# Kernel tuning notes

Hardware: AMD Instinct MI355X
Metric: run time of the kernel (lower is better)

The kernel has to match this reference:

```python
import jax, jax.numpy as jnp
import numpy as np

B, D = 8192, 1024          # batch, input dim
UNITS = [1024, 512]        # expert MLP hidden sizes
T, E_T, E_S = 2, 2, 4      # num_tasks, experts per task, shared experts
E = T * E_T + E_S          # total experts = 8


def setup_inputs() -> dict:
    key = jax.random.key(0)
    k = jax.random.split(key, 6)
    H, O = UNITS
    x = jax.random.normal(k[0], (B, D), dtype=jnp.float32)
    # glorot-normal-ish scaling for expert weights
    W1 = jax.random.normal(k[1], (E, D, H), dtype=jnp.float32) * np.sqrt(2.0 / (D + H))
    b1 = jnp.zeros((E, H), dtype=jnp.float32)
    W2 = jax.random.normal(k[2], (E, H, O), dtype=jnp.float32) * np.sqrt(2.0 / (H + O))
    b2 = jnp.zeros((E, O), dtype=jnp.float32)
    # per-task gate over (E_T + E_S) experts, no bias (use_bias=False in Dense)
    Wg = jax.random.normal(k[3], (T, D, E_T + E_S), dtype=jnp.float32) * np.sqrt(2.0 / (D + E_T + E_S))
    # shared gate over all E experts
    Wgs = jax.random.normal(k[4], (D, E), dtype=jnp.float32) * np.sqrt(2.0 / (D + E))
    return {"x": x, "W1": W1, "b1": b1, "W2": W2, "b2": b2, "Wg": Wg, "Wgs": Wgs}


def reference(x, W1, b1, W2, b2, Wg, Wgs):
    # All experts see the same input (2D-input path of CGC3: tf.tile over experts).
    # Batched grouped GEMM over the expert axis instead of a Python loop.
    h = jax.nn.relu(jnp.einsum('bd,edh->ebh', x, W1) + b1[:, None, :])   # [E,B,H]
    eo = jax.nn.relu(jnp.einsum('ebh,eho->ebo', h, W2) + b2[:, None, :]) # [E,B,O]

    outs = []
    for i in range(T):
        # experts for task i = its own E_T experts + the last E_S shared experts
        idx = jnp.array(list(range(i * E_T, (i + 1) * E_T)) + list(range(E - E_S, E)))
        g = jax.nn.softmax(x @ Wg[i], axis=-1)            # [B, E_T+E_S]
        sel = eo[idx]                                     # [E_T+E_S, B, O]
        outs.append(jnp.einsum('be,ebo->bo', g, sel))     # [B, O]
    # output_share=True: share tower gated over all experts
    gs = jax.nn.softmax(x @ Wgs, axis=-1)                 # [B, E]
    outs.append(jnp.einsum('be,ebo->bo', gs, eo))         # [B, O]
    return jnp.stack(outs, axis=1)                        # [B, T+1, O]
```

## Files before the change

kernel.cpp:

```cpp
#include <hip/hip_runtime.h>
#include <hip/hip_bf16.h>
#include <stdint.h>

#define B_SZ 8192
#define D_SZ 1024
#define H_SZ 1024
#define O_SZ 512
#define E_SZ 8

typedef float f32x4 __attribute__((ext_vector_type(4)));
typedef __bf16 bf16x8 __attribute__((ext_vector_type(8)));

typedef __attribute__((address_space(1))) uint32_t gu32;
typedef __attribute__((address_space(3))) uint32_t lu32;

__device__ __forceinline__ unsigned short f2bf(float f) {
    union { __hip_bfloat16 h; unsigned short u; } c;
    c.h = __float2bfloat16(f);
    return c.u;
}
__device__ __forceinline__ float bf2f(unsigned short u) {
    union { float f; uint32_t u; } c;
    c.u = ((uint32_t)u) << 16;
    return c.f;
}

__global__ __launch_bounds__(256) void k_convert(const float* __restrict__ in,
                                                 unsigned short* __restrict__ out, int n8) {
    int i = blockIdx.x * 256 + threadIdx.x;
    if (i >= n8) return;
    const float4* p = (const float4*)in + (size_t)i * 2;
    float4 a = p[0], b = p[1];
    ushort4 lo, hi;
    lo.x = f2bf(a.x); lo.y = f2bf(a.y); lo.z = f2bf(a.z); lo.w = f2bf(a.w);
    hi.x = f2bf(b.x); hi.y = f2bf(b.y); hi.z = f2bf(b.z); hi.w = f2bf(b.w);
    ushort4* q = (ushort4*)out + (size_t)i * 2;
    q[0] = lo; q[1] = hi;
}

__global__ __launch_bounds__(512) void k_transpose_convert(const float* __restrict__ in,
                                                           unsigned short* __restrict__ out,
                                                           int R, int C) {
    __shared__ float tile[64][65];
    const float* src = in + (size_t)blockIdx.z * R * C;
    unsigned short* dst = out + (size_t)blockIdx.z * R * C;
    int c0 = blockIdx.x * 64, r0 = blockIdx.y * 64;
    int tx = threadIdx.x, ty = threadIdx.y;
#pragma unroll
    for (int rr = ty; rr < 64; rr += 8)
        tile[rr][tx] = src[(size_t)(r0 + rr) * C + c0 + tx];
    __syncthreads();
#pragma unroll
    for (int rr = ty; rr < 64; rr += 8)
        dst[(size_t)(c0 + rr) * R + r0 + tx] = f2bf(tile[tx][rr]);
}

__global__ __launch_bounds__(256) void k_gates(const float* __restrict__ x,
                                               const float* __restrict__ Wg,
                                               const float* __restrict__ Wgs,
                                               float* __restrict__ g_all) {
    const int wv = threadIdx.x >> 6;
    const int lane = threadIdx.x & 63;
    const int b = blockIdx.x * 4 + wv;
    const float* xr = x + (size_t)b * D_SZ;
    float acc[20];
#pragma unroll
    for (int j = 0; j < 20; ++j) acc[j] = 0.f;
    for (int d = lane; d < D_SZ; d += 64) {
        float xv = xr[d];
        const float* w0 = Wg + (size_t)d * 6;
        const float* w1 = Wg + (size_t)D_SZ * 6 + (size_t)d * 6;
        const float* ws = Wgs + (size_t)d * 8;
#pragma unroll
        for (int j = 0; j < 6; ++j) acc[j] += xv * w0[j];
#pragma unroll
        for (int j = 0; j < 6; ++j) acc[6 + j] += xv * w1[j];
#pragma unroll
        for (int j = 0; j < 8; ++j) acc[12 + j] += xv * ws[j];
    }
#pragma unroll
    for (int j = 0; j < 20; ++j) {
        float v = acc[j];
#pragma unroll
        for (int s = 32; s > 0; s >>= 1) v += __shfl_down(v, s, 64);
        acc[j] = v;
    }
    if (lane == 0) {
        float* g = g_all + (size_t)b * 20;
#pragma unroll
        for (int t = 0; t < 3; ++t) {
            int base = (t == 0) ? 0 : (t == 1 ? 6 : 12);
            int cnt  = (t == 2) ? 8 : 6;
            float m = -1e30f;
            for (int j = 0; j < cnt; ++j) m = fmaxf(m, acc[base + j]);
            float ex[8]; float sum = 0.f;
            for (int j = 0; j < cnt; ++j) { ex[j] = __expf(acc[base + j] - m); sum += ex[j]; }
            float inv = 1.f / sum;
            for (int j = 0; j < cnt; ++j) g[base + j] = ex[j] * inv;
        }
    }
}

__global__ __launch_bounds__(512, 2) void k_gemm4(
    const unsigned short* __restrict__ A,
    const unsigned short* __restrict__ Bt,
    const float* __restrict__ bias,
    unsigned short* __restrict__ C,
    int M, int N, int K,
    long long sA, long long sB, long long sBias, long long sC, int e_base) {

    const int tid = threadIdx.x;
    const int lane = tid & 63, wid = tid >> 6;
    const int wr = wid >> 2, wc = wid & 3;
    const int lr = lane & 15, lg = lane >> 4;

    const int nwg = gridDim.x;
    const int wg = blockIdx.x;
    const int swz = (wg & 7) * (nwg >> 3) + (wg >> 3);
    const int nx = N >> 8;
    const int my = M >> 8;
    const int bx = swz % nx;
    const int t1 = swz / nx;
    const int by = t1 % my;
    const int e  = t1 / my + e_base;

    A    += (size_t)((long long)e * sA);
    Bt   += (size_t)((long long)e * sB);
    bias += (size_t)((long long)e * sBias);
    C    += (size_t)((long long)e * sC);

    const int m0 = by * 256, n0 = bx * 256;

    __shared__ __align__(16) unsigned short lds[65536];
    char* ldsb = (char*)lds;

    const int srow = tid >> 2;
    const int scol = (((tid & 3) ^ ((tid >> 3) & 3)) * 8);
    const int sdst = tid * 16;

    auto stageA = [&](int t) {
        const int bb = (t & 3) * 32768;
        const unsigned short* s0 = A + (size_t)(m0 + srow) * K + (t << 5) + scol;
        __builtin_amdgcn_global_load_lds((gu32*)s0, (lu32*)(ldsb + bb + sdst), 16, 0, 0);
        __builtin_amdgcn_global_load_lds((gu32*)(s0 + (size_t)128 * K),
                                         (lu32*)(ldsb + bb + 8192 + sdst), 16, 0, 0);
    };
    auto stageB = [&](int t) {
        const int bb = (t & 3) * 32768 + 16384;
        const unsigned short* s0 = Bt + (size_t)(n0 + srow) * K + (t << 5) + scol;
        __builtin_amdgcn_global_load_lds((gu32*)s0, (lu32*)(ldsb + bb + sdst), 16, 0, 0);
        __builtin_amdgcn_global_load_lds((gu32*)(s0 + (size_t)128 * K),
                                         (lu32*)(ldsb + bb + 8192 + sdst), 16, 0, 0);
    };

    const int cblk = (lg ^ ((lr >> 1) & 3)) * 16;
    const int aoff = wr * 8192 + lr * 64 + cblk;
    const int boff = 16384 + (wc >> 1) * 8192 + (wc & 1) * 4096 + lr * 64 + cblk;

    auto loadf = [&](bf16x8* f, int bb) {
#pragma unroll
        for (int i = 0; i < 8; ++i)
            f[i] = *(const bf16x8*)(ldsb + bb + aoff + i * 1024);
#pragma unroll
        for (int j = 0; j < 4; ++j)
            f[8 + j] = *(const bf16x8*)(ldsb + bb + boff + j * 1024);
    };

    f32x4 acc[8][4];
#pragma unroll
    for (int i = 0; i < 8; ++i)
#pragma unroll
        for (int j = 0; j < 4; ++j)
            acc[i][j] = f32x4{0.f, 0.f, 0.f, 0.f};

    auto domfma = [&](const bf16x8* f) {
        __builtin_amdgcn_s_setprio(1);
#pragma unroll
        for (int i = 0; i < 8; ++i)
#pragma unroll
            for (int j = 0; j < 4; ++j)
                acc[i][j] = __builtin_amdgcn_mfma_f32_16x16x32_bf16(f[i], f[8 + j], acc[i][j], 0, 0, 0);
        __builtin_amdgcn_s_setprio(0);
    };

    const int NT = K >> 5;

    stageA(0); stageB(0); stageA(1); stageB(1); stageA(2); stageB(2);
    asm volatile("s_waitcnt vmcnt(4)" ::: "memory");
    asm volatile("s_barrier" ::: "memory");

    bf16x8 fA[12], fB[12];
    loadf(fA, 0);

    for (int t = 0; t < NT; t += 2) {
        if (t + 3 < NT) { stageA(t + 3); stageB(t + 3); }
        loadf(fB, ((t + 1) & 3) * 32768);
        domfma(fA);
        if (t + 3 < NT)      { asm volatile("s_waitcnt vmcnt(4)" ::: "memory"); }
        else if (t + 2 < NT) { asm volatile("s_waitcnt vmcnt(0)" ::: "memory"); }
        asm volatile("s_barrier" ::: "memory");

        if (t + 4 < NT) { stageA(t + 4); stageB(t + 4); }
        if (t + 2 < NT) loadf(fA, ((t + 2) & 3) * 32768);
        domfma(fB);
        if (t + 4 < NT)      { asm volatile("s_waitcnt vmcnt(4)" ::: "memory"); }
        else if (t + 3 < NT) { asm volatile("s_waitcnt vmcnt(0)" ::: "memory"); }
        asm volatile("s_barrier" ::: "memory");
    }

    unsigned short* ct = (unsigned short*)ldsb;
#pragma unroll
    for (int j = 0; j < 4; ++j) {
        const int nn = wc * 64 + j * 16 + lr;
        const float bv = bias[n0 + nn];
#pragma unroll
        for (int i = 0; i < 8; ++i) {
            const int mb = wr * 128 + i * 16 + lg * 4;
#pragma unroll
            for (int r = 0; r < 4; ++r) {
                float v = fmaxf(acc[i][j][r] + bv, 0.f);
                ct[(size_t)(mb + r) * 256 + nn] = f2bf(v);
            }
        }
    }
    __syncthreads();
#pragma unroll
    for (int it = 0; it < 16; ++it) {
        const int row = it * 16 + (tid >> 5);
        const int colE = (tid & 31) * 8;
        *(int4*)(&C[(size_t)(m0 + row) * N + n0 + colE]) =
            *(const int4*)(ldsb + it * 8192 + (size_t)tid * 16);
    }
}

__global__ __launch_bounds__(256) void k_combine(const unsigned short* __restrict__ eo,
                                                 const float* __restrict__ g_all,
                                                 float* __restrict__ out) {
    int idx4 = blockIdx.x * 256 + threadIdx.x;
    int b = idx4 >> 7;
    int o4 = (idx4 & 127) * 4;
    const float* g = g_all + (size_t)b * 20;
    float v[E_SZ][4];
#pragma unroll
    for (int e = 0; e < E_SZ; ++e) {
        ushort4 u = *(const ushort4*)(eo + (size_t)e * B_SZ * O_SZ + (size_t)b * O_SZ + o4);
        v[e][0] = bf2f(u.x); v[e][1] = bf2f(u.y); v[e][2] = bf2f(u.z); v[e][3] = bf2f(u.w);
    }
    float4 r0, r1, r2;
    float* p0 = (float*)&r0; float* p1 = (float*)&r1; float* p2 = (float*)&r2;
#pragma unroll
    for (int c = 0; c < 4; ++c) {
        p0[c] = g[0] * v[0][c] + g[1] * v[1][c] + g[2] * v[4][c] + g[3] * v[5][c]
              + g[4] * v[6][c] + g[5] * v[7][c];
        p1[c] = g[6] * v[2][c] + g[7] * v[3][c] + g[8] * v[4][c] + g[9] * v[5][c]
              + g[10] * v[6][c] + g[11] * v[7][c];
        float s = 0.f;
#pragma unroll
        for (int e = 0; e < E_SZ; ++e) s += g[12 + e] * v[e][c];
        p2[c] = s;
    }
    size_t ob = (size_t)b * (3 * O_SZ) + o4;
    *(float4*)(out + ob) = r0;
    *(float4*)(out + ob + O_SZ) = r1;
    *(float4*)(out + ob + 2 * O_SZ) = r2;
}

extern "C" void kernel_launch(void* const* d_in, const int* in_sizes, int n_in,
                              void* d_out, int out_size, void* d_ws, size_t ws_size,
                              hipStream_t stream) {
    const float* x   = (const float*)d_in[0];
    const float* W1  = (const float*)d_in[1];
    const float* b1  = (const float*)d_in[2];
    const float* W2  = (const float*)d_in[3];
    const float* b2  = (const float*)d_in[4];
    const float* Wg  = (const float*)d_in[5];
    const float* Wgs = (const float*)d_in[6];
    float* out = (float*)d_out;

    char* ws = (char*)d_ws;
    const size_t SZ_XBF  = (size_t)B_SZ * D_SZ * 2;
    const size_t SZ_W1T  = (size_t)E_SZ * H_SZ * D_SZ * 2;
    const size_t SZ_W2T  = (size_t)E_SZ * O_SZ * H_SZ * 2;
    const size_t SZ_EO   = (size_t)E_SZ * B_SZ * O_SZ * 2;
    const size_t SZ_G    = (size_t)B_SZ * 20 * 4;
    const size_t SZ_HBIG = (size_t)E_SZ * B_SZ * H_SZ * 2;

    unsigned short* x_bf = (unsigned short*)ws;              ws += SZ_XBF;
    unsigned short* W1T  = (unsigned short*)ws;              ws += SZ_W1T;
    unsigned short* W2T  = (unsigned short*)ws;              ws += SZ_W2T;
    unsigned short* eo   = (unsigned short*)ws;              ws += SZ_EO;
    float* g_all         = (float*)ws;                       ws += SZ_G;
    unsigned short* h_buf = (unsigned short*)ws;

    const size_t fixed = SZ_XBF + SZ_W1T + SZ_W2T + SZ_EO + SZ_G;
    const bool big = ws_size >= fixed + SZ_HBIG;

    k_convert<<<(B_SZ * D_SZ / 8 + 255) / 256, 256, 0, stream>>>(x, x_bf, B_SZ * D_SZ / 8);
    dim3 tb(64, 8);
    k_transpose_convert<<<dim3(H_SZ / 64, D_SZ / 64, E_SZ), tb, 0, stream>>>(W1, W1T, D_SZ, H_SZ);
    k_transpose_convert<<<dim3(O_SZ / 64, H_SZ / 64, E_SZ), tb, 0, stream>>>(W2, W2T, H_SZ, O_SZ);

    k_gates<<<B_SZ / 4, 256, 0, stream>>>(x, Wg, Wgs, g_all);

    if (big) {
        k_gemm4<<<(H_SZ / 256) * (B_SZ / 256) * E_SZ, 512, 0, stream>>>(
            x_bf, W1T, b1, h_buf, B_SZ, H_SZ, D_SZ,
            0LL, (long long)H_SZ * D_SZ, (long long)H_SZ, (long long)B_SZ * H_SZ, 0);
        k_gemm4<<<(O_SZ / 256) * (B_SZ / 256) * E_SZ, 512, 0, stream>>>(
            h_buf, W2T, b2, eo, B_SZ, O_SZ, H_SZ,
            (long long)B_SZ * H_SZ, (long long)O_SZ * H_SZ, (long long)O_SZ, (long long)B_SZ * O_SZ, 0);
    } else {
        for (int e = 0; e < E_SZ; ++e) {
            k_gemm4<<<(H_SZ / 256) * (B_SZ / 256), 512, 0, stream>>>(
                x_bf, W1T, b1, h_buf, B_SZ, H_SZ, D_SZ,
                0LL, (long long)H_SZ * D_SZ, (long long)H_SZ, 0LL, e);
            k_gemm4<<<(O_SZ / 256) * (B_SZ / 256), 512, 0, stream>>>(
                h_buf, W2T, b2, eo, B_SZ, O_SZ, H_SZ,
                0LL, (long long)O_SZ * H_SZ, (long long)O_SZ, (long long)B_SZ * O_SZ, e);
        }
    }

    k_combine<<<(B_SZ * O_SZ / 4) / 256, 256, 0, stream>>>(eo, g_all, out);
}
```

Before: 305.7 us.

## Switch GEMM to 32x32x16 MFMA tiles and fuse x conversion into gate kernel

The GEMM inner product moves from 16x16x32 MFMA instructions to 32x32x16 ones, with the fragment loads, accumulator layout and epilogue row mapping reworked to match. Larger MFMA tiles cut the instruction count and the LDS fragment reads per FLOP. Separately, the bf16 conversion of x is folded into the gate kernel, so x is read once and one launch is removed. The new epilogue index mapping must match the 32x32 output layout exactly, and the gate loop now reads x with float4 loads.

```diff
diff --git a/kernel.cpp b/kernel.cpp
--- a/kernel.cpp
+++ b/kernel.cpp
@@ -9,6 +9,7 @@
 #define E_SZ 8
 
 typedef float f32x4 __attribute__((ext_vector_type(4)));
+typedef float f32x16 __attribute__((ext_vector_type(16)));
 typedef __bf16 bf16x8 __attribute__((ext_vector_type(8)));
 
 typedef __attribute__((address_space(1))) uint32_t gu32;
@@ -25,58 +26,41 @@
     return c.f;
 }
 
-__global__ __launch_bounds__(256) void k_convert(const float* __restrict__ in,
-                                                 unsigned short* __restrict__ out, int n8) {
-    int i = blockIdx.x * 256 + threadIdx.x;
-    if (i >= n8) return;
-    const float4* p = (const float4*)in + (size_t)i * 2;
-    float4 a = p[0], b = p[1];
-    ushort4 lo, hi;
-    lo.x = f2bf(a.x); lo.y = f2bf(a.y); lo.z = f2bf(a.z); lo.w = f2bf(a.w);
-    hi.x = f2bf(b.x); hi.y = f2bf(b.y); hi.z = f2bf(b.z); hi.w = f2bf(b.w);
-    ushort4* q = (ushort4*)out + (size_t)i * 2;
-    q[0] = lo; q[1] = hi;
-}
-
-__global__ __launch_bounds__(512) void k_transpose_convert(const float* __restrict__ in,
-                                                           unsigned short* __restrict__ out,
-                                                           int R, int C) {
-    __shared__ float tile[64][65];
-    const float* src = in + (size_t)blockIdx.z * R * C;
-    unsigned short* dst = out + (size_t)blockIdx.z * R * C;
-    int c0 = blockIdx.x * 64, r0 = blockIdx.y * 64;
-    int tx = threadIdx.x, ty = threadIdx.y;
-#pragma unroll
-    for (int rr = ty; rr < 64; rr += 8)
-        tile[rr][tx] = src[(size_t)(r0 + rr) * C + c0 + tx];
-    __syncthreads();
-#pragma unroll
-    for (int rr = ty; rr < 64; rr += 8)
-        dst[(size_t)(c0 + rr) * R + r0 + tx] = f2bf(tile[tx][rr]);
-}
-
-__global__ __launch_bounds__(256) void k_gates(const float* __restrict__ x,
-                                               const float* __restrict__ Wg,
-                                               const float* __restrict__ Wgs,
-                                               float* __restrict__ g_all) {
+__global__ __launch_bounds__(256) void k_convert_gates(const float* __restrict__ x,
+                                                       const float* __restrict__ Wg,
+                                                       const float* __restrict__ Wgs,
+                                                       unsigned short* __restrict__ x_bf,
+                                                       float* __restrict__ g_all) {
     const int wv = threadIdx.x >> 6;
     const int lane = threadIdx.x & 63;
     const int b = blockIdx.x * 4 + wv;
     const float* xr = x + (size_t)b * D_SZ;
+    unsigned short* xo = x_bf + (size_t)b * D_SZ;
     float acc[20];
 #pragma unroll
     for (int j = 0; j < 20; ++j) acc[j] = 0.f;
-    for (int d = lane; d < D_SZ; d += 64) {
-        float xv = xr[d];
-        const float* w0 = Wg + (size_t)d * 6;
-        const float* w1 = Wg + (size_t)D_SZ * 6 + (size_t)d * 6;
-        const float* ws = Wgs + (size_t)d * 8;
-#pragma unroll
-        for (int j = 0; j < 6; ++j) acc[j] += xv * w0[j];
-#pragma unroll
-        for (int j = 0; j < 6; ++j) acc[6 + j] += xv * w1[j];
-#pragma unroll
-        for (int j = 0; j < 8; ++j) acc[12 + j] += xv * ws[j];
+#pragma unroll
+    for (int it = 0; it < 4; ++it) {
+        const int d0 = (it * 64 + lane) * 4;
+        float4 xv = *(const float4*)(xr + d0);
+        ushort4 o;
+        o.x = f2bf(xv.x); o.y = f2bf(xv.y); o.z = f2bf(xv.z); o.w = f2bf(xv.w);
+        *(ushort4*)(xo + d0) = o;
+        const float* pv = (const float*)&xv;
+#pragma unroll
+        for (int c = 0; c < 4; ++c) {
+            const int d = d0 + c;
+            const float v = pv[c];
+            const float* w0 = Wg + (size_t)d * 6;
+            const float* w1 = Wg + (size_t)D_SZ * 6 + (size_t)d * 6;
+            const float* ws = Wgs + (size_t)d * 8;
+#pragma unroll
+            for (int j = 0; j < 6; ++j) acc[j] += v * w0[j];
+#pragma unroll
+            for (int j = 0; j < 6; ++j) acc[6 + j] += v * w1[j];
+#pragma unroll
+            for (int j = 0; j < 8; ++j) acc[12 + j] += v * ws[j];
+        }
     }
 #pragma unroll
     for (int j = 0; j < 20; ++j) {
@@ -101,6 +85,23 @@
     }
 }
 
+__global__ __launch_bounds__(512) void k_transpose_convert(const float* __restrict__ in,
+                                                           unsigned short* __restrict__ out,
+                                                           int R, int C) {
+    __shared__ float tile[64][65];
+    const float* src = in + (size_t)blockIdx.z * R * C;
+    unsigned short* dst = out + (size_t)blockIdx.z * R * C;
+    int c0 = blockIdx.x * 64, r0 = blockIdx.y * 64;
+    int tx = threadIdx.x, ty = threadIdx.y;
+#pragma unroll
+    for (int rr = ty; rr < 64; rr += 8)
+        tile[rr][tx] = src[(size_t)(r0 + rr) * C + c0 + tx];
+    __syncthreads();
+#pragma unroll
+    for (int rr = ty; rr < 64; rr += 8)
+        dst[(size_t)(c0 + rr) * R + r0 + tx] = f2bf(tile[tx][rr]);
+}
+
 __global__ __launch_bounds__(512, 2) void k_gemm4(
     const unsigned short* __restrict__ A,
     const unsigned short* __restrict__ Bt,
@@ -112,7 +113,7 @@
     const int tid = threadIdx.x;
     const int lane = tid & 63, wid = tid >> 6;
     const int wr = wid >> 2, wc = wid & 3;
-    const int lr = lane & 15, lg = lane >> 4;
+    const int lr32 = lane & 31, hi = lane >> 5;
 
     const int nwg = gridDim.x;
     const int wg = blockIdx.x;
@@ -153,33 +154,43 @@
                                          (lu32*)(ldsb + bb + 8192 + sdst), 16, 0, 0);
     };
 
-    const int cblk = (lg ^ ((lr >> 1) & 3)) * 16;
-    const int aoff = wr * 8192 + lr * 64 + cblk;
-    const int boff = 16384 + (wc >> 1) * 8192 + (wc & 1) * 4096 + lr * 64 + cblk;
+    const int sxor = (lr32 >> 1) & 3;
+    const int cblk0 = ((0 * 2 + hi) ^ sxor) * 16;
+    const int cblk1 = ((1 * 2 + hi) ^ sxor) * 16;
+    const int aoff = wr * 8192 + lr32 * 64;
+    const int boff = 16384 + (wc >> 1) * 8192 + (wc & 1) * 4096 + lr32 * 64;
 
     auto loadf = [&](bf16x8* f, int bb) {
 #pragma unroll
-        for (int i = 0; i < 8; ++i)
-            f[i] = *(const bf16x8*)(ldsb + bb + aoff + i * 1024);
-#pragma unroll
-        for (int j = 0; j < 4; ++j)
-            f[8 + j] = *(const bf16x8*)(ldsb + bb + boff + j * 1024);
+        for (int mi = 0; mi < 4; ++mi) {
+            f[mi * 2 + 0] = *(const bf16x8*)(ldsb + bb + aoff + mi * 2048 + cblk0);
+            f[mi * 2 + 1] = *(const bf16x8*)(ldsb + bb + aoff + mi * 2048 + cblk1);
+        }
+#pragma unroll
+        for (int nj = 0; nj < 2; ++nj) {
+            f[8 + nj * 2 + 0] = *(const bf16x8*)(ldsb + bb + boff + nj * 2048 + cblk0);
+            f[8 + nj * 2 + 1] = *(const bf16x8*)(ldsb + bb + boff + nj * 2048 + cblk1);
+        }
     };
 
-    f32x4 acc[8][4];
-#pragma unroll
-    for (int i = 0; i < 8; ++i)
-#pragma unroll
-        for (int j = 0; j < 4; ++j)
-            acc[i][j] = f32x4{0.f, 0.f, 0.f, 0.f};
+    f32x16 acc[4][2];
+#pragma unroll
+    for (int i = 0; i < 4; ++i)
+#pragma unroll
+        for (int j = 0; j < 2; ++j)
+            acc[i][j] = (f32x16)(0.f);
 
     auto domfma = [&](const bf16x8* f) {
         __builtin_amdgcn_s_setprio(1);
 #pragma unroll
-        for (int i = 0; i < 8; ++i)
-#pragma unroll
-            for (int j = 0; j < 4; ++j)
-                acc[i][j] = __builtin_amdgcn_mfma_f32_16x16x32_bf16(f[i], f[8 + j], acc[i][j], 0, 0, 0);
+        for (int mi = 0; mi < 4; ++mi)
+#pragma unroll
+            for (int nj = 0; nj < 2; ++nj) {
+                acc[mi][nj] = __builtin_amdgcn_mfma_f32_32x32x16_bf16(
+                    f[mi * 2 + 0], f[8 + nj * 2 + 0], acc[mi][nj], 0, 0, 0);
+                acc[mi][nj] = __builtin_amdgcn_mfma_f32_32x32x16_bf16(
+                    f[mi * 2 + 1], f[8 + nj * 2 + 1], acc[mi][nj], 0, 0, 0);
+            }
         __builtin_amdgcn_s_setprio(0);
     };
 
@@ -210,16 +221,16 @@
 
     unsigned short* ct = (unsigned short*)ldsb;
 #pragma unroll
-    for (int j = 0; j < 4; ++j) {
-        const int nn = wc * 64 + j * 16 + lr;
+    for (int nj = 0; nj < 2; ++nj) {
+        const int nn = wc * 64 + nj * 32 + lr32;
         const float bv = bias[n0 + nn];
 #pragma unroll
-        for (int i = 0; i < 8; ++i) {
-            const int mb = wr * 128 + i * 16 + lg * 4;
-#pragma unroll
-            for (int r = 0; r < 4; ++r) {
-                float v = fmaxf(acc[i][j][r] + bv, 0.f);
-                ct[(size_t)(mb + r) * 256 + nn] = f2bf(v);
+        for (int mi = 0; mi < 4; ++mi) {
+#pragma unroll
+            for (int r = 0; r < 16; ++r) {
+                const int mloc = wr * 128 + mi * 32 + (r & 3) + 8 * (r >> 2) + 4 * hi;
+                float v = fmaxf(acc[mi][nj][r] + bv, 0.f);
+                ct[(size_t)mloc * 256 + nn] = f2bf(v);
             }
         }
     }
@@ -295,12 +306,10 @@
     const size_t fixed = SZ_XBF + SZ_W1T + SZ_W2T + SZ_EO + SZ_G;
     const bool big = ws_size >= fixed + SZ_HBIG;
 
-    k_convert<<<(B_SZ * D_SZ / 8 + 255) / 256, 256, 0, stream>>>(x, x_bf, B_SZ * D_SZ / 8);
+    k_convert_gates<<<B_SZ / 4, 256, 0, stream>>>(x, Wg, Wgs, x_bf, g_all);
     dim3 tb(64, 8);
     k_transpose_convert<<<dim3(H_SZ / 64, D_SZ / 64, E_SZ), tb, 0, stream>>>(W1, W1T, D_SZ, H_SZ);
     k_transpose_convert<<<dim3(O_SZ / 64, H_SZ / 64, E_SZ), tb, 0, stream>>>(W2, W2T, H_SZ, O_SZ);
-
-    k_gates<<<B_SZ / 4, 256, 0, stream>>>(x, Wg, Wgs, g_all);
 
     if (big) {
         k_gemm4<<<(H_SZ / 256) * (B_SZ / 256) * E_SZ, 512, 0, stream>>>(
```

Result: slower. 351.5 us (+15.0%).

## Use 4-wave GEMM blocks with 128x128 per-wave tiles and fuse x conversion into gates

Applied to the files above, without the earlier changes.

The GEMM kernel drops from 512 to 256 threads per block. Each wave now computes a 128x128 sub-tile with 64 accumulators instead of 128x64, so each LDS fragment load feeds more MFMAs. Staging is merged into one lambda issuing 8 async loads per thread, and the setprio hints are removed. Separately, the fp32-to-bf16 conversion of x is folded into the gating kernel, which saves a launch and a second read of x. The trade-off is much higher register pressure and fewer waves per CU to hide latency.

```diff
diff --git a/kernel.cpp b/kernel.cpp
--- a/kernel.cpp
+++ b/kernel.cpp
@@ -25,49 +25,24 @@
     return c.f;
 }
 
-__global__ __launch_bounds__(256) void k_convert(const float* __restrict__ in,
-                                                 unsigned short* __restrict__ out, int n8) {
-    int i = blockIdx.x * 256 + threadIdx.x;
-    if (i >= n8) return;
-    const float4* p = (const float4*)in + (size_t)i * 2;
-    float4 a = p[0], b = p[1];
-    ushort4 lo, hi;
-    lo.x = f2bf(a.x); lo.y = f2bf(a.y); lo.z = f2bf(a.z); lo.w = f2bf(a.w);
-    hi.x = f2bf(b.x); hi.y = f2bf(b.y); hi.z = f2bf(b.z); hi.w = f2bf(b.w);
-    ushort4* q = (ushort4*)out + (size_t)i * 2;
-    q[0] = lo; q[1] = hi;
-}
-
-__global__ __launch_bounds__(512) void k_transpose_convert(const float* __restrict__ in,
-                                                           unsigned short* __restrict__ out,
-                                                           int R, int C) {
-    __shared__ float tile[64][65];
-    const float* src = in + (size_t)blockIdx.z * R * C;
-    unsigned short* dst = out + (size_t)blockIdx.z * R * C;
-    int c0 = blockIdx.x * 64, r0 = blockIdx.y * 64;
-    int tx = threadIdx.x, ty = threadIdx.y;
-#pragma unroll
-    for (int rr = ty; rr < 64; rr += 8)
-        tile[rr][tx] = src[(size_t)(r0 + rr) * C + c0 + tx];
-    __syncthreads();
-#pragma unroll
-    for (int rr = ty; rr < 64; rr += 8)
-        dst[(size_t)(c0 + rr) * R + r0 + tx] = f2bf(tile[tx][rr]);
-}
-
-__global__ __launch_bounds__(256) void k_gates(const float* __restrict__ x,
-                                               const float* __restrict__ Wg,
-                                               const float* __restrict__ Wgs,
-                                               float* __restrict__ g_all) {
+__global__ __launch_bounds__(256) void k_convert_gates(const float* __restrict__ x,
+                                                       const float* __restrict__ Wg,
+                                                       const float* __restrict__ Wgs,
+                                                       unsigned short* __restrict__ x_bf,
+                                                       float* __restrict__ g_all) {
     const int wv = threadIdx.x >> 6;
     const int lane = threadIdx.x & 63;
     const int b = blockIdx.x * 4 + wv;
     const float* xr = x + (size_t)b * D_SZ;
+    unsigned short* xo = x_bf + (size_t)b * D_SZ;
     float acc[20];
 #pragma unroll
     for (int j = 0; j < 20; ++j) acc[j] = 0.f;
-    for (int d = lane; d < D_SZ; d += 64) {
-        float xv = xr[d];
+#pragma unroll 4
+    for (int it = 0; it < 16; ++it) {
+        const int d = it * 64 + lane;
+        const float xv = xr[d];
+        xo[d] = f2bf(xv);
         const float* w0 = Wg + (size_t)d * 6;
         const float* w1 = Wg + (size_t)D_SZ * 6 + (size_t)d * 6;
         const float* ws = Wgs + (size_t)d * 8;
@@ -101,7 +76,24 @@
     }
 }
 
-__global__ __launch_bounds__(512, 2) void k_gemm4(
+__global__ __launch_bounds__(512) void k_transpose_convert(const float* __restrict__ in,
+                                                           unsigned short* __restrict__ out,
+                                                           int R, int C) {
+    __shared__ float tile[64][65];
+    const float* src = in + (size_t)blockIdx.z * R * C;
+    unsigned short* dst = out + (size_t)blockIdx.z * R * C;
+    int c0 = blockIdx.x * 64, r0 = blockIdx.y * 64;
+    int tx = threadIdx.x, ty = threadIdx.y;
+#pragma unroll
+    for (int rr = ty; rr < 64; rr += 8)
+        tile[rr][tx] = src[(size_t)(r0 + rr) * C + c0 + tx];
+    __syncthreads();
+#pragma unroll
+    for (int rr = ty; rr < 64; rr += 8)
+        dst[(size_t)(c0 + rr) * R + r0 + tx] = f2bf(tile[tx][rr]);
+}
+
+__global__ __launch_bounds__(256, 1) void k_gemm4(
     const unsigned short* __restrict__ A,
     const unsigned short* __restrict__ Bt,
     const float* __restrict__ bias,
@@ -111,7 +103,7 @@
 
     const int tid = threadIdx.x;
     const int lane = tid & 63, wid = tid >> 6;
-    const int wr = wid >> 2, wc = wid & 3;
+    const int wr = wid >> 1, wc = wid & 1;
     const int lr = lane & 15, lg = lane >> 4;
 
     const int nwg = gridDim.x;
@@ -138,80 +130,77 @@
     const int scol = (((tid & 3) ^ ((tid >> 3) & 3)) * 8);
     const int sdst = tid * 16;
 
-    auto stageA = [&](int t) {
+    auto stage = [&](int t) {
         const int bb = (t & 3) * 32768;
-        const unsigned short* s0 = A + (size_t)(m0 + srow) * K + (t << 5) + scol;
-        __builtin_amdgcn_global_load_lds((gu32*)s0, (lu32*)(ldsb + bb + sdst), 16, 0, 0);
-        __builtin_amdgcn_global_load_lds((gu32*)(s0 + (size_t)128 * K),
-                                         (lu32*)(ldsb + bb + 8192 + sdst), 16, 0, 0);
-    };
-    auto stageB = [&](int t) {
-        const int bb = (t & 3) * 32768 + 16384;
-        const unsigned short* s0 = Bt + (size_t)(n0 + srow) * K + (t << 5) + scol;
-        __builtin_amdgcn_global_load_lds((gu32*)s0, (lu32*)(ldsb + bb + sdst), 16, 0, 0);
-        __builtin_amdgcn_global_load_lds((gu32*)(s0 + (size_t)128 * K),
-                                         (lu32*)(ldsb + bb + 8192 + sdst), 16, 0, 0);
+        const unsigned short* a0 = A + (size_t)(m0 + srow) * K + (t << 5) + scol;
+        const unsigned short* b0 = Bt + (size_t)(n0 + srow) * K + (t << 5) + scol;
+#pragma unroll
+        for (int r = 0; r < 4; ++r)
+            __builtin_amdgcn_global_load_lds((gu32*)(a0 + (size_t)(r * 64) * K),
+                                             (lu32*)(ldsb + bb + r * 4096 + sdst), 16, 0, 0);
+#pragma unroll
+        for (int r = 0; r < 4; ++r)
+            __builtin_amdgcn_global_load_lds((gu32*)(b0 + (size_t)(r * 64) * K),
+                                             (lu32*)(ldsb + bb + 16384 + r * 4096 + sdst), 16, 0, 0);
     };
 
     const int cblk = (lg ^ ((lr >> 1) & 3)) * 16;
     const int aoff = wr * 8192 + lr * 64 + cblk;
-    const int boff = 16384 + (wc >> 1) * 8192 + (wc & 1) * 4096 + lr * 64 + cblk;
+    const int boff = 16384 + wc * 8192 + lr * 64 + cblk;
 
     auto loadf = [&](bf16x8* f, int bb) {
 #pragma unroll
         for (int i = 0; i < 8; ++i)
             f[i] = *(const bf16x8*)(ldsb + bb + aoff + i * 1024);
 #pragma unroll
-        for (int j = 0; j < 4; ++j)
+        for (int j = 0; j < 8; ++j)
             f[8 + j] = *(const bf16x8*)(ldsb + bb + boff + j * 1024);
     };
 
-    f32x4 acc[8][4];
+    f32x4 acc[8][8];
 #pragma unroll
     for (int i = 0; i < 8; ++i)
 #pragma unroll
-        for (int j = 0; j < 4; ++j)
+        for (int j = 0; j < 8; ++j)
             acc[i][j] = f32x4{0.f, 0.f, 0.f, 0.f};
 
     auto domfma = [&](const bf16x8* f) {
-        __builtin_amdgcn_s_setprio(1);
 #pragma unroll
         for (int i = 0; i < 8; ++i)
 #pragma unroll
-            for (int j = 0; j < 4; ++j)
+            for (int j = 0; j < 8; ++j)
                 acc[i][j] = __builtin_amdgcn_mfma_f32_16x16x32_bf16(f[i], f[8 + j], acc[i][j], 0, 0, 0);
-        __builtin_amdgcn_s_setprio(0);
     };
 
     const int NT = K >> 5;
 
-    stageA(0); stageB(0); stageA(1); stageB(1); stageA(2); stageB(2);
-    asm volatile("s_waitcnt vmcnt(4)" ::: "memory");
+    stage(0); stage(1); stage(2);
+    asm volatile("s_waitcnt vmcnt(8)" ::: "memory");
     asm volatile("s_barrier" ::: "memory");
 
-    bf16x8 fA[12], fB[12];
+    bf16x8 fA[16], fB[16];
     loadf(fA, 0);
 
     for (int t = 0; t < NT; t += 2) {
-        if (t + 3 < NT) { stageA(t + 3); stageB(t + 3); }
+        if (t + 3 < NT) stage(t + 3);
         loadf(fB, ((t + 1) & 3) * 32768);
         domfma(fA);
-        if (t + 3 < NT)      { asm volatile("s_waitcnt vmcnt(4)" ::: "memory"); }
+        if (t + 3 < NT)      { asm volatile("s_waitcnt vmcnt(8)" ::: "memory"); }
         else if (t + 2 < NT) { asm volatile("s_waitcnt vmcnt(0)" ::: "memory"); }
         asm volatile("s_barrier" ::: "memory");
 
-        if (t + 4 < NT) { stageA(t + 4); stageB(t + 4); }
+        if (t + 4 < NT) stage(t + 4);
         if (t + 2 < NT) loadf(fA, ((t + 2) & 3) * 32768);
         domfma(fB);
-        if (t + 4 < NT)      { asm volatile("s_waitcnt vmcnt(4)" ::: "memory"); }
+        if (t + 4 < NT)      { asm volatile("s_waitcnt vmcnt(8)" ::: "memory"); }
         else if (t + 3 < NT) { asm volatile("s_waitcnt vmcnt(0)" ::: "memory"); }
         asm volatile("s_barrier" ::: "memory");
     }
 
     unsigned short* ct = (unsigned short*)ldsb;
 #pragma unroll
-    for (int j = 0; j < 4; ++j) {
-        const int nn = wc * 64 + j * 16 + lr;
+    for (int j = 0; j < 8; ++j) {
+        const int nn = wc * 128 + j * 16 + lr;
         const float bv = bias[n0 + nn];
 #pragma unroll
         for (int i = 0; i < 8; ++i) {
@@ -225,11 +214,11 @@
     }
     __syncthreads();
 #pragma unroll
-    for (int it = 0; it < 16; ++it) {
-        const int row = it * 16 + (tid >> 5);
+    for (int it = 0; it < 32; ++it) {
+        const int row = it * 8 + (tid >> 5);
         const int colE = (tid & 31) * 8;
         *(int4*)(&C[(size_t)(m0 + row) * N + n0 + colE]) =
-            *(const int4*)(ldsb + it * 8192 + (size_t)tid * 16);
+            *(const int4*)(ldsb + it * 4096 + (size_t)tid * 16);
     }
 }
 
@@ -295,26 +284,24 @@
     const size_t fixed = SZ_XBF + SZ_W1T + SZ_W2T + SZ_EO + SZ_G;
     const bool big = ws_size >= fixed + SZ_HBIG;
 
-    k_convert<<<(B_SZ * D_SZ / 8 + 255) / 256, 256, 0, stream>>>(x, x_bf, B_SZ * D_SZ / 8);
+    k_convert_gates<<<B_SZ / 4, 256, 0, stream>>>(x, Wg, Wgs, x_bf, g_all);
     dim3 tb(64, 8);
     k_transpose_convert<<<dim3(H_SZ / 64, D_SZ / 64, E_SZ), tb, 0, stream>>>(W1, W1T, D_SZ, H_SZ);
     k_transpose_convert<<<dim3(O_SZ / 64, H_SZ / 64, E_SZ), tb, 0, stream>>>(W2, W2T, H_SZ, O_SZ);
 
-    k_gates<<<B_SZ / 4, 256, 0, stream>>>(x, Wg, Wgs, g_all);
-
     if (big) {
-        k_gemm4<<<(H_SZ / 256) * (B_SZ / 256) * E_SZ, 512, 0, stream>>>(
+        k_gemm4<<<(H_SZ / 256) * (B_SZ / 256) * E_SZ, 256, 0, stream>>>(
             x_bf, W1T, b1, h_buf, B_SZ, H_SZ, D_SZ,
             0LL, (long long)H_SZ * D_SZ, (long long)H_SZ, (long long)B_SZ * H_SZ, 0);
-        k_gemm4<<<(O_SZ / 256) * (B_SZ / 256) * E_SZ, 512, 0, stream>>>(
+        k_gemm4<<<(O_SZ / 256) * (B_SZ / 256) * E_SZ, 256, 0, stream>>>(
             h_buf, W2T, b2, eo, B_SZ, O_SZ, H_SZ,
             (long long)B_SZ * H_SZ, (long long)O_SZ * H_SZ, (long long)O_SZ, (long long)B_SZ * O_SZ, 0);
     } else {
         for (int e = 0; e < E_SZ; ++e) {
-            k_gemm4<<<(H_SZ / 256) * (B_SZ / 256), 512, 0, stream>>>(
+            k_gemm4<<<(H_SZ / 256) * (B_SZ / 256), 256, 0, stream>>>(
                 x_bf, W1T, b1, h_buf, B_SZ, H_SZ, D_SZ,
                 0LL, (long long)H_SZ * D_SZ, (long long)H_SZ, 0LL, e);
-            k_gemm4<<<(O_SZ / 256) * (B_SZ / 256), 512, 0, stream>>>(
+            k_gemm4<<<(O_SZ / 256) * (B_SZ / 256), 256, 0, stream>>>(
                 h_buf, W2T, b2, eo, B_SZ, O_SZ, H_SZ,
                 0LL, (long long)O_SZ * H_SZ, (long long)O_SZ, (long long)B_SZ * O_SZ, e);
         }
```

New measurement: 403.2 us. 1.32x slower.
